# Performance work log

Measured on AMD Instinct MI355X. Metric: run time of the kernel, lower is better.

The kernel has to match this reference:

```python
import jax, jax.numpy as jnp
import numpy as np

N_NODES = 500_000
HIDDEN = 128
REDUCED = HIDDEN // 2
N_GRAPHS = 4096


def setup_inputs() -> dict:
    key = jax.random.key(0)
    k_x, k_b, k_w1, k_w2 = jax.random.split(key, 4)
    x = jax.random.normal(k_x, (N_NODES, HIDDEN), dtype=jnp.float32)
    batch = jnp.sort(jax.random.randint(k_b, (N_NODES,), 0, N_GRAPHS, dtype=jnp.int64))
    # Xavier-uniform init like the torch module; biases zero.
    lim1 = float(np.sqrt(6.0 / (HIDDEN + REDUCED)))
    lim2 = float(np.sqrt(6.0 / (REDUCED + HIDDEN)))
    W1 = jax.random.uniform(k_w1, (HIDDEN, REDUCED), minval=-lim1, maxval=lim1, dtype=jnp.float32)
    b1 = jnp.zeros((REDUCED,), dtype=jnp.float32)
    W2 = jax.random.uniform(k_w2, (REDUCED, HIDDEN), minval=-lim2, maxval=lim2, dtype=jnp.float32)
    b2 = jnp.zeros((HIDDEN,), dtype=jnp.float32)
    return {"x": x, "batch": batch, "size": N_GRAPHS, "W1": W1, "b1": b1, "W2": W2, "b2": b2}


def reference(x, batch, size, W1, b1, W2, b2):
    # scatter-sum pool over graphs: [G, H]
    pooled = jax.ops.segment_sum(x, batch, num_segments=size)
    # squeeze-excite MLP + sigmoid gate
    h = jax.nn.relu(pooled @ W1 + b1)          # [G, H/2]
    y = jax.nn.sigmoid(h @ W2 + b2)            # [G, H]
    # gather-broadcast gate back to nodes and modulate features
    return x * y[batch]                        # [N, H]
```

## Files before the change

kernel.cpp:

```cpp
#include <hip/hip_runtime.h>

#define HIDDEN  128
#define REDUCED 64
#define NGRAPHS 4096

typedef float f4 __attribute__((ext_vector_type(4)));

__global__ void pool_mlp_kernel(const float* __restrict__ x,
                                const int* __restrict__ batch,
                                const float* __restrict__ W1, const float* __restrict__ b1,
                                const float* __restrict__ W2, const float* __restrict__ b2,
                                float* __restrict__ y, int n_nodes) {
    const int g = blockIdx.x;
    const int t = threadIdx.x;
    __shared__ int s_range[2];
    if (t == 0) {
        int lo = 0, hi = n_nodes;
        while (lo < hi) { int mid = (lo + hi) >> 1; if (batch[mid] <  g) lo = mid + 1; else hi = mid; }
        s_range[0] = lo;
    } else if (t == 64) {
        int lo = 0, hi = n_nodes;
        while (lo < hi) { int mid = (lo + hi) >> 1; if (batch[mid] <= g) lo = mid + 1; else hi = mid; }
        s_range[1] = lo;
    }
    __syncthreads();
    const int lo = s_range[0], hi = s_range[1];
    const int r = t >> 5, c = t & 31;

    f4 acc = {0.f, 0.f, 0.f, 0.f};
    for (int n = lo + r; n < hi; n += 4) {
        const f4 v = ((const f4*)(x + (size_t)n * HIDDEN))[c];
        acc += v;
    }
    __shared__ f4 red[4][32];
    __shared__ float p_s[HIDDEN];
    __shared__ float h_s[REDUCED];
    red[r][c] = acc;
    __syncthreads();
    if (r == 0) {
        const f4 a = red[0][c], b = red[1][c], d = red[2][c], e = red[3][c];
        f4 s;
        s.x = a.x + b.x + d.x + e.x;
        s.y = a.y + b.y + d.y + e.y;
        s.z = a.z + b.z + d.z + e.z;
        s.w = a.w + b.w + d.w + e.w;
        ((f4*)p_s)[c] = s;
    }
    __syncthreads();

    if (t < REDUCED) {
        float a1 = b1[t];
        #pragma unroll 8
        for (int i = 0; i < HIDDEN; ++i) a1 = fmaf(p_s[i], W1[i * REDUCED + t], a1);
        h_s[t] = a1 > 0.f ? a1 : 0.f;
    }
    __syncthreads();
    float a2 = b2[t];
    #pragma unroll 8
    for (int j = 0; j < REDUCED; ++j) a2 = fmaf(h_s[j], W2[j * HIDDEN + t], a2);
    y[(size_t)g * HIDDEN + t] = 1.f / (1.f + __expf(-a2));
}

__global__ void modulate_kernel(const float* __restrict__ x,
                                const int* __restrict__ batch,
                                const float* __restrict__ y,
                                float* __restrict__ out, long long total4) {
    const long long idx = (long long)blockIdx.x * blockDim.x + threadIdx.x;
    if (idx >= total4) return;
    const long long n = idx >> 5;
    const int c = (int)(idx & 31);
    const int g = batch[n];
    const f4 xv = __builtin_nontemporal_load((const f4*)x + idx);
    const f4 yv = ((const f4*)y)[(size_t)g * (HIDDEN / 4) + c];
    f4 o;
    o.x = xv.x * yv.x; o.y = xv.y * yv.y; o.z = xv.z * yv.z; o.w = xv.w * yv.w;
    __builtin_nontemporal_store(o, (f4*)out + idx);
}

extern "C" void kernel_launch(void* const* d_in, const int* in_sizes, int n_in,
                              void* d_out, int out_size, void* d_ws, size_t ws_size,
                              hipStream_t stream) {
    const float* x     = (const float*)d_in[0];
    const int*   batch = (const int*)d_in[1];
    const float* W1 = (const float*)d_in[3];
    const float* b1 = (const float*)d_in[4];
    const float* W2 = (const float*)d_in[5];
    const float* b2 = (const float*)d_in[6];
    float* out = (float*)d_out;

    const int n_nodes = in_sizes[0] / HIDDEN;

    float* y = (float*)d_ws;

    pool_mlp_kernel<<<NGRAPHS, 128, 0, stream>>>(x, batch, W1, b1, W2, b2, y, n_nodes);

    const long long total4 = (long long)n_nodes * (HIDDEN / 4);
    const int blocks = (int)((total4 + 255) / 256);
    modulate_kernel<<<blocks, 256, 0, stream>>>(x, batch, y, out, total4);
}
```

Measured before the change: 485.2 us.

## Fuse pooling, MLP and modulation into one kernel with register-buffered node rows

```diff
diff --git a/kernel.cpp b/kernel.cpp
--- a/kernel.cpp
+++ b/kernel.cpp
@@ -3,14 +3,16 @@
 #define HIDDEN  128
 #define REDUCED 64
 #define NGRAPHS 4096
+#define BUF_IT  24
 
 typedef float f4 __attribute__((ext_vector_type(4)));
 
-__global__ void pool_mlp_kernel(const float* __restrict__ x,
-                                const int* __restrict__ batch,
-                                const float* __restrict__ W1, const float* __restrict__ b1,
-                                const float* __restrict__ W2, const float* __restrict__ b2,
-                                float* __restrict__ y, int n_nodes) {
+__global__ void __launch_bounds__(256, 2)
+fused_kernel(const float* __restrict__ x,
+             const int* __restrict__ batch,
+             const float* __restrict__ W1, const float* __restrict__ b1,
+             const float* __restrict__ W2, const float* __restrict__ b2,
+             float* __restrict__ out, int n_nodes) {
     const int g = blockIdx.x;
     const int t = threadIdx.x;
     __shared__ int s_range[2];
@@ -27,23 +29,32 @@
     const int lo = s_range[0], hi = s_range[1];
     const int r = t >> 5, c = t & 31;
 
+    f4 buf[BUF_IT];
     f4 acc = {0.f, 0.f, 0.f, 0.f};
-    for (int n = lo + r; n < hi; n += 4) {
-        const f4 v = ((const f4*)(x + (size_t)n * HIDDEN))[c];
-        acc += v;
+    const f4* __restrict__ x4 = (const f4*)x;
+    #pragma unroll
+    for (int i = 0; i < BUF_IT; ++i) {
+        const int n = lo + r + 8 * i;
+        if (n < hi) {
+            const f4 v = __builtin_nontemporal_load(x4 + (size_t)n * 32 + c);
+            buf[i] = v;
+            acc += v;
+        }
     }
-    __shared__ f4 red[4][32];
+    for (int n = lo + r + 8 * BUF_IT; n < hi; n += 8) {
+        acc += x4[(size_t)n * 32 + c];
+    }
+
+    __shared__ f4 red[8][32];
     __shared__ float p_s[HIDDEN];
     __shared__ float h_s[REDUCED];
+    __shared__ float y_s[HIDDEN];
     red[r][c] = acc;
     __syncthreads();
     if (r == 0) {
-        const f4 a = red[0][c], b = red[1][c], d = red[2][c], e = red[3][c];
-        f4 s;
-        s.x = a.x + b.x + d.x + e.x;
-        s.y = a.y + b.y + d.y + e.y;
-        s.z = a.z + b.z + d.z + e.z;
-        s.w = a.w + b.w + d.w + e.w;
+        f4 s = red[0][c];
+        #pragma unroll
+        for (int k = 1; k < 8; ++k) s += red[k][c];
         ((f4*)p_s)[c] = s;
     }
     __syncthreads();
@@ -55,26 +66,32 @@
         h_s[t] = a1 > 0.f ? a1 : 0.f;
     }
     __syncthreads();
-    float a2 = b2[t];
-    #pragma unroll 8
-    for (int j = 0; j < REDUCED; ++j) a2 = fmaf(h_s[j], W2[j * HIDDEN + t], a2);
-    y[(size_t)g * HIDDEN + t] = 1.f / (1.f + __expf(-a2));
-}
+    if (t < HIDDEN) {
+        float a2 = b2[t];
+        #pragma unroll 8
+        for (int j = 0; j < REDUCED; ++j) a2 = fmaf(h_s[j], W2[j * HIDDEN + t], a2);
+        y_s[t] = 1.f / (1.f + __expf(-a2));
+    }
+    __syncthreads();
 
-__global__ void modulate_kernel(const float* __restrict__ x,
-                                const int* __restrict__ batch,
-                                const float* __restrict__ y,
-                                float* __restrict__ out, long long total4) {
-    const long long idx = (long long)blockIdx.x * blockDim.x + threadIdx.x;
-    if (idx >= total4) return;
-    const long long n = idx >> 5;
-    const int c = (int)(idx & 31);
-    const int g = batch[n];
-    const f4 xv = __builtin_nontemporal_load((const f4*)x + idx);
-    const f4 yv = ((const f4*)y)[(size_t)g * (HIDDEN / 4) + c];
-    f4 o;
-    o.x = xv.x * yv.x; o.y = xv.y * yv.y; o.z = xv.z * yv.z; o.w = xv.w * yv.w;
-    __builtin_nontemporal_store(o, (f4*)out + idx);
+    const f4 yv = ((const f4*)y_s)[c];
+    f4* __restrict__ out4 = (f4*)out;
+    #pragma unroll
+    for (int i = 0; i < BUF_IT; ++i) {
+        const int n = lo + r + 8 * i;
+        if (n < hi) {
+            const f4 v = buf[i];
+            f4 o;
+            o.x = v.x * yv.x; o.y = v.y * yv.y; o.z = v.z * yv.z; o.w = v.w * yv.w;
+            __builtin_nontemporal_store(o, out4 + (size_t)n * 32 + c);
+        }
+    }
+    for (int n = lo + r + 8 * BUF_IT; n < hi; n += 8) {
+        const f4 v = x4[(size_t)n * 32 + c];
+        f4 o;
+        o.x = v.x * yv.x; o.y = v.y * yv.y; o.z = v.z * yv.z; o.w = v.w * yv.w;
+        __builtin_nontemporal_store(o, out4 + (size_t)n * 32 + c);
+    }
 }
 
 extern "C" void kernel_launch(void* const* d_in, const int* in_sizes, int n_in,
@@ -90,11 +107,5 @@
 
     const int n_nodes = in_sizes[0] / HIDDEN;
 
-    float* y = (float*)d_ws;
-
-    pool_mlp_kernel<<<NGRAPHS, 128, 0, stream>>>(x, batch, W1, b1, W2, b2, y, n_nodes);
-
-    const long long total4 = (long long)n_nodes * (HIDDEN / 4);
-    const int blocks = (int)((total4 + 255) / 256);
-    modulate_kernel<<<blocks, 256, 0, stream>>>(x, batch, y, out, total4);
+    fused_kernel<<<NGRAPHS, 256, 0, stream>>>(x, batch, W1, b1, W2, b2, out, n_nodes);
 }
```

New measurement: 633.7 us. +30.6%, slower.
